# Kernel tuning notes

Hardware: AMD Instinct MI355X
Metric: run time of the kernel (lower is better)

The kernel has to match this reference:

```python
import jax, jax.numpy as jnp
import numpy as np

N = 100000      # nodes
E = 1600000     # edges (avg degree 16)
IN_F, HID, OUT_F, NC = 384, 128, 64, 2
EPS = 1e-5
NEG_SLOPE = 0.01


def _layernorm(x, g, b):
    m = jnp.mean(x, axis=-1, keepdims=True)
    v = jnp.var(x, axis=-1, keepdims=True)
    return (x - m) * jax.lax.rsqrt(v + EPS) * g + b


def _graph_conv(x, edge_index, edge_weight, w_rel, b_rel, w_root):
    # PyG GraphConv: lin_rel(scatter_add(w_e * x[src] -> dst)) + lin_root(x)
    src, dst = edge_index[0], edge_index[1]
    msg = x[src] * edge_weight[:, None]                      # [E, C]
    agg = jax.ops.segment_sum(msg, dst, num_segments=x.shape[0])  # [N, C]
    return agg @ w_rel.T + b_rel + x @ w_root.T


def _xavier(key, shape):
    fan_in, fan_out = shape[1], shape[0]
    lim = float(np.sqrt(6.0 / (fan_in + fan_out)))
    return jax.random.uniform(key, shape, jnp.float32, -lim, lim)


def setup_inputs() -> dict:
    key = jax.random.key(0)
    ks = jax.random.split(key, 10)
    x = jax.random.normal(ks[0], (N, IN_F), jnp.float32)
    edge_index = jax.random.randint(ks[1], (2, E), 0, N, jnp.int64)
    edge_attr = jax.random.uniform(ks[2], (E,), jnp.float32)
    return {
        "x": x,
        "edge_index": edge_index,
        "edge_attr": edge_attr,
        "ln1_g": jnp.ones((IN_F,), jnp.float32),
        "ln1_b": jnp.zeros((IN_F,), jnp.float32),
        "fc1_w": _xavier(ks[3], (HID, IN_F)),
        "fc1_b": jnp.zeros((HID,), jnp.float32),
        "c1_wrel": _xavier(ks[4], (HID, HID)),
        "c1_brel": jnp.zeros((HID,), jnp.float32),
        "c1_wroot": _xavier(ks[5], (HID, HID)),
        "c2_wrel": _xavier(ks[6], (OUT_F, HID)),
        "c2_brel": jnp.zeros((OUT_F,), jnp.float32),
        "c2_wroot": _xavier(ks[7], (OUT_F, HID)),
        "ln2_g": jnp.ones((OUT_F,), jnp.float32),
        "ln2_b": jnp.zeros((OUT_F,), jnp.float32),
        "fc2_w": _xavier(ks[8], (NC, OUT_F)),
        "fc2_b": jnp.zeros((NC,), jnp.float32),
    }


def reference(x, edge_index, edge_attr,
              ln1_g, ln1_b, fc1_w, fc1_b,
              c1_wrel, c1_brel, c1_wroot,
              c2_wrel, c2_brel, c2_wroot,
              ln2_g, ln2_b, fc2_w, fc2_b):
    h = _layernorm(x, ln1_g, ln1_b) @ fc1_w.T + fc1_b          # [N, HID]
    h = _graph_conv(h, edge_index, edge_attr, c1_wrel, c1_brel, c1_wroot)
    h = jax.nn.leaky_relu(h, NEG_SLOPE)
    h = _graph_conv(h, edge_index, edge_attr, c2_wrel, c2_brel, c2_wroot)
    h = jax.nn.leaky_relu(h, NEG_SLOPE)                        # [N, OUT_F]
    out = _layernorm(h, ln2_g, ln2_b) @ fc2_w.T + fc2_b        # [N, NC]
    return out
```

## Files before the change

### kernel.cpp

```cpp
#include <hip/hip_runtime.h>
#include <hip/hip_bf16.h>

#define N_IN_F 384
#define N_HID  128
#define N_OUT  64

typedef unsigned short ushort_t;
typedef __attribute__((ext_vector_type(8))) short short8v;
typedef __attribute__((ext_vector_type(4))) float floatx4;

union U8 { uint4 v; unsigned short u[8]; };

__device__ __forceinline__ float bfu2f(unsigned short s){
    union { unsigned i; float f; } c; c.i = ((unsigned)s) << 16; return c.f;
}
__device__ __forceinline__ unsigned short f2bfu(float f){
    __hip_bfloat16 h = __float2bfloat16(f);
    union { __hip_bfloat16 h; unsigned short u; } c; c.h = h; return c.u;
}

__device__ __forceinline__ float loadS(const void* p, size_t i, int fm){
    return fm ? bfu2f(((const unsigned short*)p)[i]) : ((const float*)p)[i];
}

__global__ void k_detect_all(const int* __restrict__ ei, const unsigned* __restrict__ xw,
                             int* __restrict__ modep){
    int lane = threadIdx.x & 63;
    int zi = 0;
    if (lane < 32) zi = ei[2*lane + 1];
    int cnt = 0;
    #pragma unroll
    for (int q = 0; q < 8; q++){
        unsigned w = xw[lane*8 + q];
        unsigned elo = (w >> 7) & 0xff;
        cnt += (elo >= 118 && elo <= 134) ? 1 : 0;
    }
    #pragma unroll
    for (int m = 32; m; m >>= 1){ zi |= __shfl_xor(zi, m, 64); cnt += __shfl_xor(cnt, m, 64); }
    if (lane == 0 && blockIdx.x == 0){
        modep[0] = (zi == 0) ? 1 : 0;
        modep[1] = (cnt >= 256) ? 1 : 0;
    }
}

__device__ __forceinline__ int edge_src(const int* ei, int e, int i, int mode){
    return mode ? ei[2*(size_t)i] : ei[i];
}
__device__ __forceinline__ int edge_dst(const int* ei, int e, int i, int mode){
    return mode ? ei[2*(size_t)e + 2*(size_t)i] : ei[(size_t)e + i];
}

__global__ void k_hist(const int* __restrict__ ei, int e, int n, const int* __restrict__ modep,
                       int* __restrict__ deg, unsigned* __restrict__ rel){
    int i = blockIdx.x * 256 + threadIdx.x;
    if (i >= e) return;
    int mode = modep[0];
    int d = edge_dst(ei, e, i, mode);
    if ((unsigned)d >= (unsigned)n) return;
    rel[i] = (unsigned)atomicAdd(&deg[d], 1);
}

__global__ __launch_bounds__(1024) void k_blksum(
    const int* __restrict__ deg, int n, int* __restrict__ part)
{
    __shared__ int s[1024];
    int i = blockIdx.x * 1024 + threadIdx.x;
    s[threadIdx.x] = (i < n) ? deg[i] : 0;
    __syncthreads();
    for (int off = 512; off; off >>= 1){
        if (threadIdx.x < off) s[threadIdx.x] += s[threadIdx.x + off];
        __syncthreads();
    }
    if (threadIdx.x == 0) part[blockIdx.x] = s[0];
}

__global__ __launch_bounds__(128) void k_scanpart(
    int* __restrict__ part, int nb, int* __restrict__ rowoff, int n)
{
    __shared__ int s[128];
    int t = threadIdx.x;
    if (nb <= 128){
        int v = (t < nb) ? part[t] : 0;
        s[t] = v; __syncthreads();
        #pragma unroll
        for (int off = 1; off < 128; off <<= 1){
            int tmp = (t >= off) ? s[t - off] : 0;
            __syncthreads();
            s[t] += tmp;
            __syncthreads();
        }
        if (t < nb) part[t] = s[t] - v;
        if (t == 127) rowoff[n] = s[127];
    } else if (t == 0){
        int run = 0;
        for (int b = 0; b < nb; b++){ int tt = part[b]; part[b] = run; run += tt; }
        rowoff[n] = run;
    }
}

__global__ __launch_bounds__(1024) void k_scanblk(
    int* __restrict__ deg, const int* __restrict__ part, int n, int* __restrict__ rowoff)
{
    __shared__ int s[1024];
    int t = threadIdx.x;
    int i = blockIdx.x * 1024 + t;
    int v = (i < n) ? deg[i] : 0;
    s[t] = v; __syncthreads();
    for (int off = 1; off < 1024; off <<= 1){
        int tmp = (t >= off) ? s[t - off] : 0;
        __syncthreads();
        s[t] += tmp;
        __syncthreads();
    }
    if (i < n){
        int excl = s[t] - v + part[blockIdx.x];
        rowoff[i] = excl;
        deg[i]    = excl;
    }
}

__global__ void k_scatter(const int* __restrict__ ei, const void* __restrict__ ea,
                          int e, int n, const int* __restrict__ modep,
                          int* __restrict__ cursor, int2* __restrict__ colw)
{
    int i = blockIdx.x * 256 + threadIdx.x;
    if (i >= e) return;
    int mode = modep[0], fm = modep[1];
    int d = edge_dst(ei, e, i, mode);
    if ((unsigned)d >= (unsigned)n) return;
    int s = edge_src(ei, e, i, mode);
    if ((unsigned)s >= (unsigned)n) s = 0;
    int pos = atomicAdd(&cursor[d], 1);
    if ((unsigned)pos >= (unsigned)e) return;
    int2 pk; pk.x = s; pk.y = __float_as_int(loadS(ea, i, fm));
    colw[pos] = pk;
}

#define SC_CHUNK 2048
#define SC_BSHIFT 13
#define SC_MAXB 1024
__global__ __launch_bounds__(256) void k_scoarse(
    const int* __restrict__ ei, const void* __restrict__ ea,
    const unsigned* __restrict__ rel, const int* __restrict__ rowoff,
    const int* __restrict__ modep, int e, int n, int B,
    int4* __restrict__ tmp, int* __restrict__ off2)
{
    __shared__ int  hcnt[SC_MAXB];
    __shared__ int  hoff[SC_MAXB + 1];
    __shared__ int4 stage[SC_CHUNK];
    int t = threadIdx.x;
    int c = blockIdx.x;
    int chunk0 = c * SC_CHUNK;
    int mode = modep[0], fm = modep[1];

    for (int q = t; q < B; q += 256) hcnt[q] = 0;
    __syncthreads();

    int  pos[8], sv[8], wv[8];
    bool val[8];
    #pragma unroll
    for (int k = 0; k < 8; k++){
        int i = chunk0 + k*256 + t;
        val[k] = false;
        if (i < e){
            int d = edge_dst(ei, e, i, mode);
            if ((unsigned)d < (unsigned)n){
                int s = edge_src(ei, e, i, mode);
                if ((unsigned)s >= (unsigned)n) s = 0;
                int p = rowoff[d] + (int)rel[i];
                pos[k] = p; sv[k] = s; wv[k] = __float_as_int(loadS(ea, i, fm));
                val[k] = true;
                atomicAdd(&hcnt[p >> SC_BSHIFT], 1);
            }
        }
    }
    __syncthreads();
    if (t == 0){
        int run = 0;
        for (int q = 0; q < B; q++){ hoff[q] = run; run += hcnt[q]; }
        hoff[B] = run;
    }
    __syncthreads();
    for (int q = t; q < B; q += 256) hcnt[q] = 0;
    for (int q = t; q <= B; q += 256) off2[(size_t)c*(B+1) + q] = hoff[q];
    __syncthreads();
    #pragma unroll
    for (int k = 0; k < 8; k++){
        if (val[k]){
            int b = pos[k] >> SC_BSHIFT;
            int slot = hoff[b] + atomicAdd(&hcnt[b], 1);
            stage[slot] = make_int4(pos[k], sv[k], wv[k], 0);
        }
    }
    __syncthreads();
    int tot = hoff[B];
    for (int idx = t; idx < tot; idx += 256)
        tmp[(size_t)chunk0 + idx] = stage[idx];
}

__global__ __launch_bounds__(512) void k_sfine(
    const int4* __restrict__ tmp, const int* __restrict__ off2,
    int B, int nchunks, int2* __restrict__ colw)
{
    int b = blockIdx.x;
    int wv = threadIdx.x >> 6, lane = threadIdx.x & 63;
    const int NW = 8;
    int c = wv;
    if (c >= nchunks) return;
    int s0 = off2[(size_t)c*(B+1) + b];
    int s1 = off2[(size_t)c*(B+1) + b + 1];
    while (true){
        int cn = c + NW;
        int n0 = 0, n1 = 0;
        if (cn < nchunks){
            n0 = off2[(size_t)cn*(B+1) + b];
            n1 = off2[(size_t)cn*(B+1) + b + 1];
        }
        int len = s1 - s0;
        size_t base = (size_t)c * SC_CHUNK + s0;
        for (int k = lane; k < len; k += 64){
            int4 ent = tmp[base + k];
            colw[ent.x] = make_int2(ent.y, ent.z);
        }
        if (cn >= nchunks) break;
        c = cn; s0 = n0; s1 = n1;
    }
}

__global__ __launch_bounds__(64) void k_prep_w1(
    const void* __restrict__ W, const void* __restrict__ g, const void* __restrict__ b,
    const void* __restrict__ fc1b, const int* __restrict__ fmp,
    ushort_t* __restrict__ Wp, float* __restrict__ u, float* __restrict__ v)
{
    int fm = fmp[0];
    int j = blockIdx.x, lane = threadIdx.x;
    float su = 0.f, sv = 0.f;
    for (int k = lane; k < N_IN_F; k += 64){
        float w  = loadS(W, (size_t)j*N_IN_F + k, fm);
        float gk = loadS(g, k, fm);
        float bk = loadS(b, k, fm);
        unsigned short pw = f2bfu(gk * w);
        Wp[(size_t)j*N_IN_F + k] = pw;
        su += bfu2f(pw);
        sv += bk * w;
    }
    #pragma unroll
    for (int m = 32; m; m >>= 1){ su += __shfl_xor(su, m, 64); sv += __shfl_xor(sv, m, 64); }
    if (lane == 0){
        u[j] = su;
        v[j] = sv + loadS(fc1b, j, fm);
    }
}

__global__ void k_cvt4(const void* __restrict__ p0, const void* __restrict__ p1,
                       const void* __restrict__ p2, const void* __restrict__ p3,
                       const int* __restrict__ fmp, ushort_t* __restrict__ o)
{
    int fm = fmp[0];
    int i = blockIdx.x * 256 + threadIdx.x;
    if (i >= 49152) return;
    const void* p; int off;
    if (i < 16384)      { p = p0; off = i; }
    else if (i < 32768) { p = p1; off = i - 16384; }
    else if (i < 40960) { p = p2; off = i - 32768; }
    else                { p = p3; off = i - 40960; }
    o[i] = f2bfu(loadS(p, off, fm));
}

__global__ __launch_bounds__(256) void k_gemm1_mfma(
    const void* __restrict__ x, const int* __restrict__ fmp,
    const ushort_t* __restrict__ Wp,
    const float* __restrict__ u, const float* __restrict__ v,
    ushort_t* __restrict__ out, int n)
{
    int fm = fmp[0];
    int t = threadIdx.x;
    int wave = t >> 6, lane = t & 63;
    int r16 = lane & 15, kq = lane >> 4;
    int m0 = blockIdx.x * 64;
    int mw = m0 + wave * 16;
    int grow = min(mw + r16, n - 1);

    const ushort_t* xbf = (const ushort_t*)x + (size_t)grow*N_IN_F + kq*8;
    const float*    xf  = (const float*)x    + (size_t)grow*N_IN_F + kq*8;
    const ushort_t* wpB = Wp + (size_t)r16*N_IN_F + kq*8;

    floatx4 acc[8];
    #pragma unroll
    for (int c = 0; c < 8; c++) acc[c] = (floatx4){0.f,0.f,0.f,0.f};
    float s1 = 0.f, s2 = 0.f;

    if (fm){
        #pragma unroll
        for (int ks = 0; ks < 12; ks++){
            short8v af = *(const short8v*)(xbf + ks*32);
            #pragma unroll
            for (int q = 0; q < 8; q++){
                float f = bfu2f((unsigned short)af[q]);
                s1 += f; s2 += f*f;
            }
            #pragma unroll
            for (int ni = 0; ni < 8; ni++){
                short8v bf = *(const short8v*)(wpB + (size_t)ni*16*N_IN_F + ks*32);
                acc[ni] = __builtin_amdgcn_mfma_f32_16x16x32_bf16(af, bf, acc[ni], 0, 0, 0);
            }
        }
    } else {
        #pragma unroll
        for (int ks = 0; ks < 12; ks++){
            floatx4 p = *(const floatx4*)(xf + ks*32);
            floatx4 q4 = *(const floatx4*)(xf + ks*32 + 4);
            union { ushort_t u[8]; short8v v; } w_;
            w_.u[0]=f2bfu(p[0]); w_.u[1]=f2bfu(p[1]); w_.u[2]=f2bfu(p[2]); w_.u[3]=f2bfu(p[3]);
            w_.u[4]=f2bfu(q4[0]); w_.u[5]=f2bfu(q4[1]); w_.u[6]=f2bfu(q4[2]); w_.u[7]=f2bfu(q4[3]);
            short8v af = w_.v;
            #pragma unroll
            for (int q = 0; q < 8; q++){
                float f = bfu2f((unsigned short)af[q]);
                s1 += f; s2 += f*f;
            }
            #pragma unroll
            for (int ni = 0; ni < 8; ni++){
                short8v bf = *(const short8v*)(wpB + (size_t)ni*16*N_IN_F + ks*32);
                acc[ni] = __builtin_amdgcn_mfma_f32_16x16x32_bf16(af, bf, acc[ni], 0, 0, 0);
            }
        }
    }

    s1 += __shfl_xor(s1, 16, 64); s1 += __shfl_xor(s1, 32, 64);
    s2 += __shfl_xor(s2, 16, 64); s2 += __shfl_xor(s2, 32, 64);
    float mu = s1 * (1.f/384.f);
    float var = fmaxf(s2 * (1.f/384.f) - mu*mu, 0.f);
    float rs = rsqrtf(var + 1e-5f);

    float mm[4], rr[4];
    #pragma unroll
    for (int r = 0; r < 4; r++){
        mm[r] = __shfl(mu, kq*4 + r, 64);
        rr[r] = __shfl(rs, kq*4 + r, 64);
    }
    int ib = mw + kq*4;
    #pragma unroll
    for (int ni = 0; ni < 8; ni++){
        int j = ni*16 + r16;
        float uj = u[j], vj = v[j];
        #pragma unroll
        for (int r = 0; r < 4; r++){
            int ii = ib + r;
            float val = rr[r]*acc[ni][r] - rr[r]*mm[r]*uj + vj;
            if (ii < n) out[(size_t)ii*N_HID + j] = f2bfu(val);
        }
    }
}

__global__ __launch_bounds__(256) void k_conv1_mfma(
    const ushort_t* __restrict__ A1, const ushort_t* __restrict__ A2,
    const ushort_t* __restrict__ W1, const ushort_t* __restrict__ W2,
    const void* __restrict__ bias, const int* __restrict__ fmp,
    ushort_t* __restrict__ out, int n)
{
    int fm = fmp[0];
    int t = threadIdx.x;
    int wave = t >> 6, lane = t & 63;
    int r16 = lane & 15, kq = lane >> 4;
    int m0 = blockIdx.x * 64;
    int mw = m0 + wave * 16;
    int grow = min(mw + r16, n - 1);

    size_t aoff = (size_t)grow*N_HID + kq*8;
    size_t boff = (size_t)r16*N_HID + kq*8;

    floatx4 acc[8];
    #pragma unroll
    for (int c = 0; c < 8; c++) acc[c] = (floatx4){0.f,0.f,0.f,0.f};

    #pragma unroll
    for (int ks = 0; ks < 8; ks++){
        const ushort_t* Asrc = (ks < 4) ? A1 : A2;
        const ushort_t* Wsrc = (ks < 4) ? W1 : W2;
        int kb = (ks & 3) * 32;
        short8v af = *(const short8v*)(Asrc + aoff + kb);
        #pragma unroll
        for (int ni = 0; ni < 8; ni++){
            short8v bf = *(const short8v*)(Wsrc + boff + (size_t)ni*16*N_HID + kb);
            acc[ni] = __builtin_amdgcn_mfma_f32_16x16x32_bf16(af, bf, acc[ni], 0, 0, 0);
        }
    }

    int ib = mw + kq*4;
    #pragma unroll
    for (int ni = 0; ni < 8; ni++){
        int j = ni*16 + r16;
        float bb = loadS(bias, j, fm);
        #pragma unroll
        for (int r = 0; r < 4; r++){
            int ii = ib + r;
            float val = acc[ni][r] + bb;
            val = (val >= 0.f) ? val : 0.01f * val;
            if (ii < n) out[(size_t)ii*N_HID + j] = f2bfu(val);
        }
    }
}

__global__ __launch_bounds__(256) void k_conv2_final(
    const ushort_t* __restrict__ A1, const ushort_t* __restrict__ A2,
    const ushort_t* __restrict__ W1, const ushort_t* __restrict__ W2,
    const void* __restrict__ bias,
    const void* __restrict__ gam, const void* __restrict__ bet,
    const void* __restrict__ Wfc, const void* __restrict__ bfc,
    const int* __restrict__ fmp, void* __restrict__ out, int n)
{
    int fm = fmp[0];
    int t = threadIdx.x;
    int wave = t >> 6, lane = t & 63;
    int r16 = lane & 15, kq = lane >> 4;
    int m0 = blockIdx.x * 64;
    int mw = m0 + wave * 16;
    int grow = min(mw + r16, n - 1);

    size_t aoff = (size_t)grow*N_HID + kq*8;
    size_t boff = (size_t)r16*N_HID + kq*8;

    floatx4 acc[4];
    #pragma unroll
    for (int c = 0; c < 4; c++) acc[c] = (floatx4){0.f,0.f,0.f,0.f};

    #pragma unroll
    for (int ks = 0; ks < 8; ks++){
        const ushort_t* Asrc = (ks < 4) ? A1 : A2;
        const ushort_t* Wsrc = (ks < 4) ? W1 : W2;
        int kb = (ks & 3) * 32;
        short8v af = *(const short8v*)(Asrc + aoff + kb);
        #pragma unroll
        for (int ni = 0; ni < 4; ni++){
            short8v bf = *(const short8v*)(Wsrc + boff + (size_t)ni*16*N_HID + kb);
            acc[ni] = __builtin_amdgcn_mfma_f32_16x16x32_bf16(af, bf, acc[ni], 0, 0, 0);
        }
    }

    float b0 = loadS(bfc, 0, fm), b1 = loadS(bfc, 1, fm);
    float s[4] = {}, s2[4] = {};
    #pragma unroll
    for (int ni = 0; ni < 4; ni++){
        int j = ni*16 + r16;
        float bb = loadS(bias, j, fm);
        #pragma unroll
        for (int r = 0; r < 4; r++){
            float val = acc[ni][r] + bb;
            val = (val >= 0.f) ? val : 0.01f * val;
            acc[ni][r] = val;
            s[r] += val; s2[r] += val*val;
        }
    }
    #pragma unroll
    for (int m = 1; m < 16; m <<= 1){
        #pragma unroll
        for (int r = 0; r < 4; r++){
            s[r]  += __shfl_xor(s[r],  m, 64);
            s2[r] += __shfl_xor(s2[r], m, 64);
        }
    }
    float mu[4], rstd[4];
    #pragma unroll
    for (int r = 0; r < 4; r++){
        mu[r] = s[r] * (1.f/64.f);
        float var = fmaxf(s2[r] * (1.f/64.f) - mu[r]*mu[r], 0.f);
        rstd[r] = rsqrtf(var + 1e-5f);
    }
    float p0[4] = {}, p1[4] = {};
    #pragma unroll
    for (int ni = 0; ni < 4; ni++){
        int j = ni*16 + r16;
        float gj = loadS(gam, j, fm), bj = loadS(bet, j, fm);
        float w0 = loadS(Wfc, j, fm), w1 = loadS(Wfc, 64 + j, fm);
        #pragma unroll
        for (int r = 0; r < 4; r++){
            float zn = (acc[ni][r] - mu[r]) * rstd[r] * gj + bj;
            p0[r] += zn * w0;
            p1[r] += zn * w1;
        }
    }
    #pragma unroll
    for (int m = 1; m < 16; m <<= 1){
        #pragma unroll
        for (int r = 0; r < 4; r++){
            p0[r] += __shfl_xor(p0[r], m, 64);
            p1[r] += __shfl_xor(p1[r], m, 64);
        }
    }
    if (r16 == 0){
        #pragma unroll
        for (int r = 0; r < 4; r++){
            int ii = mw + kq*4 + r;
            if (ii >= n) continue;
            float o0 = p0[r] + b0, o1 = p1[r] + b1;
            if (fm){
                unsigned pk = ((unsigned)f2bfu(o1) << 16) | (unsigned)f2bfu(o0);
                *(unsigned*)((ushort_t*)out + (size_t)ii*2) = pk;
            } else {
                float2 f2; f2.x = o0; f2.y = o1;
                *(float2*)((float*)out + (size_t)ii*2) = f2;
            }
        }
    }
}

__global__ __launch_bounds__(256) void k_agg(
    const int* __restrict__ rowoff, const int2* __restrict__ colw,
    const ushort_t* __restrict__ src_mat,
    ushort_t* __restrict__ out, int n, int eTot)
{
    int t = threadIdx.x;
    int lane = t & 63;
    int d = blockIdx.x * 4 + (t >> 6);
    if (d >= n) return;
    int grp = lane >> 4;
    int c16 = lane & 15;
    int e0 = rowoff[d], e1 = rowoff[d+1];
    e0 = max(0, min(e0, eTot));
    e1 = max(e0, min(e1, eTot));
    float acc[8] = {};
    for (int e = e0 + grp; e < e1; e += 4){
        int2 cw = colw[e];
        int s = cw.x;
        if ((unsigned)s >= (unsigned)n) s = 0;
        float wv = __int_as_float(cw.y);
        U8 u; u.v = *(const uint4*)(src_mat + (size_t)s*N_HID + c16*8);
        #pragma unroll
        for (int q = 0; q < 8; q++) acc[q] += wv * bfu2f(u.u[q]);
    }
    #pragma unroll
    for (int q = 0; q < 8; q++){
        acc[q] += __shfl_xor(acc[q], 16, 64);
        acc[q] += __shfl_xor(acc[q], 32, 64);
    }
    if (grp == 0){
        union { ushort_t u[8]; uint4 v; } P;
        #pragma unroll
        for (int q = 0; q < 8; q++) P.u[q] = f2bfu(acc[q]);
        *(uint4*)(out + (size_t)d*N_HID + c16*8) = P.v;
    }
}

extern "C" void kernel_launch(void* const* d_in, const int* in_sizes, int n_in,
                              void* d_out, int out_size, void* d_ws, size_t ws_size,
                              hipStream_t stream)
{
    const void* x     = d_in[0];
    const int*  ei    = (const int*)d_in[1];
    const void* ea    = d_in[2];
    const void* ln1g  = d_in[3];
    const void* ln1b  = d_in[4];
    const void* fc1w  = d_in[5];
    const void* fc1b  = d_in[6];
    const void* c1rel = d_in[7];
    const void* c1bre = d_in[8];
    const void* c1roo = d_in[9];
    const void* c2rel = d_in[10];
    const void* c2bre = d_in[11];
    const void* c2roo = d_in[12];
    const void* ln2g  = d_in[13];
    const void* ln2b  = d_in[14];
    const void* fc2w  = d_in[15];
    const void* fc2b  = d_in[16];
    (void)n_in; (void)out_size; (void)ws_size;

    const int n = in_sizes[0] / N_IN_F;
    const int e = in_sizes[2];

    const int nchunks = (e + SC_CHUNK - 1) / SC_CHUNK;
    const int B = (e + (1 << SC_BSHIFT) - 1) >> SC_BSHIFT;

    char* wsp = (char*)d_ws;
    size_t off = 0;
    auto alloc = [&](size_t bytes) -> char* {
        char* p = wsp + off; off += (bytes + 255) & ~(size_t)255; return p;
    };
    int*      deg    = (int*)  alloc((size_t)n * 4);
    int*      rowoff = (int*)  alloc((size_t)(n+1) * 4);
    int*      part   = (int*)  alloc(4096);
    int*      modep  = (int*)  alloc(256);
    int2*     colw   = (int2*) alloc((size_t)e * 8);
    unsigned* rel    = (unsigned*)alloc((size_t)e * 4);
    int4*     stmp   = (int4*) alloc((size_t)e * 16);
    int*      off2   = (int*)  alloc((size_t)nchunks * (B+1) * 4);
    float*    u      = (float*)alloc(128 * 4);
    float*    v      = (float*)alloc(128 * 4);
    ushort_t* Wp     = (ushort_t*)alloc((size_t)N_HID * N_IN_F * 2);
    ushort_t* cw     = (ushort_t*)alloc((size_t)49152 * 2);
    ushort_t* h1     = (ushort_t*)alloc((size_t)n * N_HID * 2);
    ushort_t* agg1   = (ushort_t*)alloc((size_t)n * N_HID * 2);
    ushort_t* g1     = (ushort_t*)alloc((size_t)n * N_HID * 2);
    ushort_t* agg2   = h1;

    hipMemsetAsync(deg, 0, (size_t)n * 4, stream);
    k_detect_all<<<1, 64, 0, stream>>>(ei, (const unsigned*)x, modep);

    int nb = (n + 1023) / 1024;
    k_hist    <<<(e + 255) / 256, 256, 0, stream>>>(ei, e, n, modep, deg, rel);
    k_blksum  <<<nb, 1024, 0, stream>>>(deg, n, part);
    k_scanpart<<<1, 128, 0, stream>>>(part, nb, rowoff, n);
    k_scanblk <<<nb, 1024, 0, stream>>>(deg, part, n, rowoff);

    if (B <= SC_MAXB){
        k_scoarse<<<nchunks, 256, 0, stream>>>(ei, ea, rel, rowoff, modep, e, n, B, stmp, off2);
        k_sfine  <<<B, 512, 0, stream>>>(stmp, off2, B, nchunks, colw);
    } else {
        k_scatter<<<(e + 255) / 256, 256, 0, stream>>>(ei, ea, e, n, modep, deg, colw);
    }

    k_prep_w1<<<N_HID, 64, 0, stream>>>(fc1w, ln1g, ln1b, fc1b, modep + 1, Wp, u, v);
    k_cvt4   <<<(49152 + 255) / 256, 256, 0, stream>>>(c1rel, c1roo, c2rel, c2roo, modep + 1, cw);

    k_gemm1_mfma<<<(n + 63) / 64, 256, 0, stream>>>(x, modep + 1, Wp, u, v, h1, n);

    k_agg<<<(n + 3) / 4, 256, 0, stream>>>(rowoff, colw, h1, agg1, n, e);
    k_conv1_mfma<<<(n + 63) / 64, 256, 0, stream>>>(agg1, h1, cw, cw + 16384, c1bre, modep + 1, g1, n);

    k_agg<<<(n + 3) / 4, 256, 0, stream>>>(rowoff, colw, g1, agg2, n, e);
    k_conv2_final<<<(n + 63) / 64, 256, 0, stream>>>(agg2, g1, cw + 32768, cw + 40960, c2bre,
                                                     ln2g, ln2b, fc2w, fc2b, modep + 1, d_out, n);
}
```

Before: 744.0 us.

## Pre-swizzle MFMA weight fragments and stage them in LDS for dense GEMMs

Weights are written at prep time in a fragment-major order that matches the MFMA B-operand lane layout. Each GEMM block copies its weight fragments into shared memory with contiguous 16-byte loads, and every wave then reads its B operands from LDS instead of doing strided global loads. Blocks grow to 512 threads and 128 rows so each weight copy is shared by more waves. The cost is a large LDS footprint per block (up to 48KB in gemm1) plus extra barriers, which may reduce occupancy.

```diff
diff --git a/kernel.cpp b/kernel.cpp
--- a/kernel.cpp
+++ b/kernel.cpp
@@ -234,13 +234,15 @@
 {
     int fm = fmp[0];
     int j = blockIdx.x, lane = threadIdx.x;
+    int ni = j >> 4, r16 = j & 15;
     float su = 0.f, sv = 0.f;
     for (int k = lane; k < N_IN_F; k += 64){
         float w  = loadS(W, (size_t)j*N_IN_F + k, fm);
         float gk = loadS(g, k, fm);
         float bk = loadS(b, k, fm);
         unsigned short pw = f2bfu(gk * w);
-        Wp[(size_t)j*N_IN_F + k] = pw;
+        int idx = ((((k >> 5)*8 + ni)*64) + (((k >> 3) & 3) << 4) + r16)*8 + (k & 7);
+        Wp[idx] = pw;
         su += bfu2f(pw);
         sv += bk * w;
     }
@@ -259,41 +261,63 @@
     int fm = fmp[0];
     int i = blockIdx.x * 256 + threadIdx.x;
     if (i >= 49152) return;
-    const void* p; int off;
-    if (i < 16384)      { p = p0; off = i; }
-    else if (i < 32768) { p = p1; off = i - 16384; }
-    else if (i < 40960) { p = p2; off = i - 32768; }
-    else                { p = p3; off = i - 40960; }
-    o[i] = f2bfu(loadS(p, off, fm));
-}
-
-__global__ __launch_bounds__(256) void k_gemm1_mfma(
+    const void* p; int off, base, NI;
+    if (i < 16384)      { p = p0; off = i;         base = 0;     NI = 8; }
+    else if (i < 32768) { p = p1; off = i - 16384; base = 16384; NI = 8; }
+    else if (i < 40960) { p = p2; off = i - 32768; base = 32768; NI = 4; }
+    else                { p = p3; off = i - 40960; base = 40960; NI = 4; }
+    int j = off >> 7, k = off & 127;
+    int fidx = ((((k >> 5)*NI + (j >> 4))*64) + (((k >> 3) & 3) << 4) + (j & 15))*8 + (k & 7);
+    o[base + fidx] = f2bfu(loadS(p, off, fm));
+}
+
+__global__ __launch_bounds__(512) void k_gemm1_mfma(
     const void* __restrict__ x, const int* __restrict__ fmp,
     const ushort_t* __restrict__ Wp,
     const float* __restrict__ u, const float* __restrict__ v,
     ushort_t* __restrict__ out, int n)
 {
+    __shared__ ushort_t Bs[24576];
     int fm = fmp[0];
     int t = threadIdx.x;
     int wave = t >> 6, lane = t & 63;
     int r16 = lane & 15, kq = lane >> 4;
-    int m0 = blockIdx.x * 64;
+    int m0 = blockIdx.x * 128;
     int mw = m0 + wave * 16;
     int grow = min(mw + r16, n - 1);
 
     const ushort_t* xbf = (const ushort_t*)x + (size_t)grow*N_IN_F + kq*8;
     const float*    xf  = (const float*)x    + (size_t)grow*N_IN_F + kq*8;
-    const ushort_t* wpB = Wp + (size_t)r16*N_IN_F + kq*8;
 
     floatx4 acc[8];
     #pragma unroll
     for (int c = 0; c < 8; c++) acc[c] = (floatx4){0.f,0.f,0.f,0.f};
     float s1 = 0.f, s2 = 0.f;
 
-    if (fm){
-        #pragma unroll
-        for (int ks = 0; ks < 12; ks++){
-            short8v af = *(const short8v*)(xbf + ks*32);
+    #pragma unroll
+    for (int h = 0; h < 2; h++){
+        if (h) __syncthreads();
+        {
+            const uint4* src = (const uint4*)(Wp + h*24576);
+            uint4* dst = (uint4*)Bs;
+            #pragma unroll
+            for (int q = 0; q < 12; q++) dst[t + q*512] = src[t + q*512];
+        }
+        __syncthreads();
+        #pragma unroll
+        for (int ksl = 0; ksl < 6; ksl++){
+            int ks = h*6 + ksl;
+            short8v af;
+            if (fm){
+                af = *(const short8v*)(xbf + ks*32);
+            } else {
+                floatx4 p  = *(const floatx4*)(xf + ks*32);
+                floatx4 q4 = *(const floatx4*)(xf + ks*32 + 4);
+                union { ushort_t u[8]; short8v v; } w_;
+                w_.u[0]=f2bfu(p[0]);  w_.u[1]=f2bfu(p[1]);  w_.u[2]=f2bfu(p[2]);  w_.u[3]=f2bfu(p[3]);
+                w_.u[4]=f2bfu(q4[0]); w_.u[5]=f2bfu(q4[1]); w_.u[6]=f2bfu(q4[2]); w_.u[7]=f2bfu(q4[3]);
+                af = w_.v;
+            }
             #pragma unroll
             for (int q = 0; q < 8; q++){
                 float f = bfu2f((unsigned short)af[q]);
@@ -301,27 +325,7 @@
             }
             #pragma unroll
             for (int ni = 0; ni < 8; ni++){
-                short8v bf = *(const short8v*)(wpB + (size_t)ni*16*N_IN_F + ks*32);
-                acc[ni] = __builtin_amdgcn_mfma_f32_16x16x32_bf16(af, bf, acc[ni], 0, 0, 0);
-            }
-        }
-    } else {
-        #pragma unroll
-        for (int ks = 0; ks < 12; ks++){
-            floatx4 p = *(const floatx4*)(xf + ks*32);
-            floatx4 q4 = *(const floatx4*)(xf + ks*32 + 4);
-            union { ushort_t u[8]; short8v v; } w_;
-            w_.u[0]=f2bfu(p[0]); w_.u[1]=f2bfu(p[1]); w_.u[2]=f2bfu(p[2]); w_.u[3]=f2bfu(p[3]);
-            w_.u[4]=f2bfu(q4[0]); w_.u[5]=f2bfu(q4[1]); w_.u[6]=f2bfu(q4[2]); w_.u[7]=f2bfu(q4[3]);
-            short8v af = w_.v;
-            #pragma unroll
-            for (int q = 0; q < 8; q++){
-                float f = bfu2f((unsigned short)af[q]);
-                s1 += f; s2 += f*f;
-            }
-            #pragma unroll
-            for (int ni = 0; ni < 8; ni++){
-                short8v bf = *(const short8v*)(wpB + (size_t)ni*16*N_IN_F + ks*32);
+                short8v bf = *(const short8v*)(Bs + ((ksl*8 + ni)*64 + lane)*8);
                 acc[ni] = __builtin_amdgcn_mfma_f32_16x16x32_bf16(af, bf, acc[ni], 0, 0, 0);
             }
         }
@@ -353,37 +357,45 @@
     }
 }
 
-__global__ __launch_bounds__(256) void k_conv1_mfma(
+__global__ __launch_bounds__(512) void k_conv1_mfma(
     const ushort_t* __restrict__ A1, const ushort_t* __restrict__ A2,
-    const ushort_t* __restrict__ W1, const ushort_t* __restrict__ W2,
+    const ushort_t* __restrict__ W1f, const ushort_t* __restrict__ W2f,
     const void* __restrict__ bias, const int* __restrict__ fmp,
     ushort_t* __restrict__ out, int n)
 {
+    __shared__ ushort_t Bs[16384];
     int fm = fmp[0];
     int t = threadIdx.x;
     int wave = t >> 6, lane = t & 63;
     int r16 = lane & 15, kq = lane >> 4;
-    int m0 = blockIdx.x * 64;
+    int m0 = blockIdx.x * 128;
     int mw = m0 + wave * 16;
     int grow = min(mw + r16, n - 1);
-
     size_t aoff = (size_t)grow*N_HID + kq*8;
-    size_t boff = (size_t)r16*N_HID + kq*8;
 
     floatx4 acc[8];
     #pragma unroll
     for (int c = 0; c < 8; c++) acc[c] = (floatx4){0.f,0.f,0.f,0.f};
 
     #pragma unroll
-    for (int ks = 0; ks < 8; ks++){
-        const ushort_t* Asrc = (ks < 4) ? A1 : A2;
-        const ushort_t* Wsrc = (ks < 4) ? W1 : W2;
-        int kb = (ks & 3) * 32;
-        short8v af = *(const short8v*)(Asrc + aoff + kb);
-        #pragma unroll
-        for (int ni = 0; ni < 8; ni++){
-            short8v bf = *(const short8v*)(Wsrc + boff + (size_t)ni*16*N_HID + kb);
-            acc[ni] = __builtin_amdgcn_mfma_f32_16x16x32_bf16(af, bf, acc[ni], 0, 0, 0);
+    for (int h = 0; h < 2; h++){
+        if (h) __syncthreads();
+        {
+            const uint4* src = (const uint4*)(h ? W2f : W1f);
+            uint4* dst = (uint4*)Bs;
+            #pragma unroll
+            for (int q = 0; q < 8; q++) dst[t + q*512] = src[t + q*512];
+        }
+        __syncthreads();
+        const ushort_t* Asrc = h ? A2 : A1;
+        #pragma unroll
+        for (int ksl = 0; ksl < 4; ksl++){
+            short8v af = *(const short8v*)(Asrc + aoff + ksl*32);
+            #pragma unroll
+            for (int ni = 0; ni < 8; ni++){
+                short8v bf = *(const short8v*)(Bs + ((ksl*8 + ni)*64 + lane)*8);
+                acc[ni] = __builtin_amdgcn_mfma_f32_16x16x32_bf16(af, bf, acc[ni], 0, 0, 0);
+            }
         }
     }
 
@@ -402,24 +414,31 @@
     }
 }
 
-__global__ __launch_bounds__(256) void k_conv2_final(
+__global__ __launch_bounds__(512) void k_conv2_final(
     const ushort_t* __restrict__ A1, const ushort_t* __restrict__ A2,
-    const ushort_t* __restrict__ W1, const ushort_t* __restrict__ W2,
+    const ushort_t* __restrict__ Wall,
     const void* __restrict__ bias,
     const void* __restrict__ gam, const void* __restrict__ bet,
     const void* __restrict__ Wfc, const void* __restrict__ bfc,
     const int* __restrict__ fmp, void* __restrict__ out, int n)
 {
+    __shared__ ushort_t Bs[16384];
     int fm = fmp[0];
     int t = threadIdx.x;
     int wave = t >> 6, lane = t & 63;
     int r16 = lane & 15, kq = lane >> 4;
-    int m0 = blockIdx.x * 64;
+    int m0 = blockIdx.x * 128;
     int mw = m0 + wave * 16;
     int grow = min(mw + r16, n - 1);
-
     size_t aoff = (size_t)grow*N_HID + kq*8;
-    size_t boff = (size_t)r16*N_HID + kq*8;
+
+    {
+        const uint4* src = (const uint4*)Wall;
+        uint4* dst = (uint4*)Bs;
+        #pragma unroll
+        for (int q = 0; q < 8; q++) dst[t + q*512] = src[t + q*512];
+    }
+    __syncthreads();
 
     floatx4 acc[4];
     #pragma unroll
@@ -428,12 +447,12 @@
     #pragma unroll
     for (int ks = 0; ks < 8; ks++){
         const ushort_t* Asrc = (ks < 4) ? A1 : A2;
-        const ushort_t* Wsrc = (ks < 4) ? W1 : W2;
-        int kb = (ks & 3) * 32;
-        short8v af = *(const short8v*)(Asrc + aoff + kb);
+        short8v af = *(const short8v*)(Asrc + aoff + (ks & 3)*32);
+        int cbase = (ks < 4) ? 0 : 16;
         #pragma unroll
         for (int ni = 0; ni < 4; ni++){
-            short8v bf = *(const short8v*)(Wsrc + boff + (size_t)ni*16*N_HID + kb);
+            int chunk = cbase + (ks & 3)*4 + ni;
+            short8v bf = *(const short8v*)(Bs + (chunk*64 + lane)*8);
             acc[ni] = __builtin_amdgcn_mfma_f32_16x16x32_bf16(af, bf, acc[ni], 0, 0, 0);
         }
     }
@@ -612,12 +631,12 @@
     k_prep_w1<<<N_HID, 64, 0, stream>>>(fc1w, ln1g, ln1b, fc1b, modep + 1, Wp, u, v);
     k_cvt4   <<<(49152 + 255) / 256, 256, 0, stream>>>(c1rel, c1roo, c2rel, c2roo, modep + 1, cw);
 
-    k_gemm1_mfma<<<(n + 63) / 64, 256, 0, stream>>>(x, modep + 1, Wp, u, v, h1, n);
+    k_gemm1_mfma<<<(n + 127) / 128, 512, 0, stream>>>(x, modep + 1, Wp, u, v, h1, n);
 
     k_agg<<<(n + 3) / 4, 256, 0, stream>>>(rowoff, colw, h1, agg1, n, e);
-    k_conv1_mfma<<<(n + 63) / 64, 256, 0, stream>>>(agg1, h1, cw, cw + 16384, c1bre, modep + 1, g1, n);
+    k_conv1_mfma<<<(n + 127) / 128, 512, 0, stream>>>(agg1, h1, cw, cw + 16384, c1bre, modep + 1, g1, n);
 
     k_agg<<<(n + 3) / 4, 256, 0, stream>>>(rowoff, colw, g1, agg2, n, e);
-    k_conv2_final<<<(n + 63) / 64, 256, 0, stream>>>(agg2, g1, cw + 32768, cw + 40960, c2bre,
-                                                     ln2g, ln2b, fc2w, fc2b, modep + 1, d_out, n);
-}
+    k_conv2_final<<<(n + 127) / 128, 512, 0, stream>>>(agg2, g1, cw + 32768, c2bre,
+                                                       ln2g, ln2b, fc2w, fc2b, modep + 1, d_out, n);
+}
```

Result: faster. 628.3 us (-15.5%).
